# Optimization experiments

Measured on AMD Instinct MI355X. Metric: run time of the kernel, lower is better.

The kernel has to match this reference:

```python
import jax, jax.numpy as jnp
import numpy as np

TAU = 1.5
K = 4
EPS = 1e-5
GN_GROUPS = 8

def conv2d(x, w, pad, rhs_dilation=(1, 1)):
    return jax.lax.conv_general_dilated(
        x, w, window_strides=(1, 1),
        padding=[(pad, pad), (pad, pad)],
        rhs_dilation=rhs_dilation,
        dimension_numbers=("NCHW", "OIHW", "NCHW"))

def setup_inputs() -> dict:
    key = jax.random.key(0)
    ks = jax.random.split(key, 16)
    s = 0.05  # weight scale to keep activations sane
    B, C, H, W = 16, 128, 64, 64
    O, HID, CG, SE = 128, 32, 16, 16
    d = {}
    d["x"] = jax.random.normal(ks[0], (B, C, H, W), jnp.float32)
    d["base_weight"] = jax.random.normal(ks[1], (O, C, 3, 3), jnp.float32) * s
    d["delta_weight"] = jax.random.normal(ks[2], (K, O, C, 3, 3), jnp.float32) * s
    d["kernel_scale"] = jnp.ones((K, O, 1, 1, 1), jnp.float32)
    d["gc_w1"] = jax.random.normal(ks[3], (HID, C), jnp.float32) * s
    d["gc_w2"] = jax.random.normal(ks[4], (C, HID), jnp.float32) * s
    d["rc_w"] = jax.random.normal(ks[5], (HID, C, 3, 3), jnp.float32) * s
    d["bn_gamma"] = jnp.ones((HID,), jnp.float32)
    d["bn_beta"] = jnp.zeros((HID,), jnp.float32)
    d["bn_mean"] = jnp.zeros((HID,), jnp.float32)
    d["bn_var"] = jnp.ones((HID,), jnp.float32)
    d["rg_w"] = jax.random.normal(ks[6], (HID, C), jnp.float32) * s
    d["gate_w"] = jax.random.normal(ks[7], (K * O, HID), jnp.float32) * s
    d["gate_b"] = jnp.zeros((K * O,), jnp.float32)
    d["cg_w1"] = jax.random.normal(ks[8], (CG, C), jnp.float32) * s
    d["cg_b1"] = jnp.zeros((CG,), jnp.float32)
    d["cg_w2"] = jax.random.normal(ks[9], (C, CG), jnp.float32) * s
    d["cg_b2"] = jnp.zeros((C,), jnp.float32)
    d["sg_w"] = jax.random.normal(ks[10], (1, 2, 7, 7), jnp.float32) * s
    d["gn_gamma"] = jnp.ones((O,), jnp.float32)
    d["gn_beta"] = jnp.zeros((O,), jnp.float32)
    d["se_w1"] = jax.random.normal(ks[11], (SE, O), jnp.float32) * s
    d["se_b1"] = jnp.zeros((SE,), jnp.float32)
    d["se_w2"] = jax.random.normal(ks[12], (O, SE), jnp.float32) * s
    d["se_b2"] = jnp.zeros((O,), jnp.float32)
    d["identity_scale"] = jnp.float32(0.0)
    d["bias"] = jnp.zeros((O,), jnp.float32)
    return d

def reference(x, base_weight, delta_weight, kernel_scale, gc_w1, gc_w2, rc_w,
              bn_gamma, bn_beta, bn_mean, bn_var, rg_w, gate_w, gate_b,
              cg_w1, cg_b1, cg_w2, cg_b2, sg_w, gn_gamma, gn_beta,
              se_w1, se_b1, se_w2, se_b2, identity_scale, bias):
    identity = x
    B, C, H, W = x.shape
    O = base_weight.shape[0]

    # global context gate (squeeze-excite style)
    p = x.mean((2, 3))                                    # [B,C]
    g = jax.nn.sigmoid(jax.nn.silu(p @ gc_w1.T) @ gc_w2.T)
    x = x * g[:, :, None, None]

    # channel gate
    pc = x.mean((2, 3))
    c_attn = jax.nn.sigmoid(jax.nn.silu(pc @ cg_w1.T + cg_b1) @ cg_w2.T + cg_b2)
    # spatial gate
    s_in = jnp.concatenate([x.mean(1, keepdims=True), x.max(1, keepdims=True)], axis=1)
    s_attn = jax.nn.sigmoid(conv2d(s_in, sg_w, pad=3))
    x = x * c_attn[:, :, None, None] * s_attn

    # router: dilated conv + BN(eval) + SiLU, plus global branch
    lf = conv2d(x, rc_w, pad=2, rhs_dilation=(2, 2))
    lf = (lf - bn_mean[None, :, None, None]) * jax.lax.rsqrt(bn_var + EPS)[None, :, None, None]
    lf = lf * bn_gamma[None, :, None, None] + bn_beta[None, :, None, None]
    lf = jax.nn.silu(lf)
    gf = jax.nn.silu(x.mean((2, 3)) @ rg_w.T)             # [B,HID]
    lf = lf + gf[:, :, None, None]
    alpha = jnp.einsum("bhij,oh->boij", lf, gate_w) + gate_b[None, :, None, None]
    alpha = alpha.reshape(B, K, O, H, W)
    alpha = jax.nn.softmax(alpha / TAU, axis=1)

    # unfold (k=3, stride=1, pad=1, dilation=1) -> H_out=H, W_out=W
    xp = jnp.pad(x, ((0, 0), (0, 0), (1, 1), (1, 1)))
    patches = jnp.stack([xp[:, :, i:i + H, j:j + W]
                         for i in range(3) for j in range(3)], axis=2)  # [B,C,9,H,W]
    L = H * W
    xu = patches.reshape(B, C * 9, L).transpose(0, 2, 1)  # [B,L,C*9]

    base = base_weight.reshape(O, -1)
    delta = (delta_weight * kernel_scale).reshape(K, O, -1)
    # same-size bilinear resize of alpha is the identity
    alpha_map = alpha.reshape(B, K, O, L)

    static = jnp.einsum("blf,of->bol", xu, base)          # [B,O,L]
    res = jnp.einsum("blf,kof->bkol", xu, delta)          # [B,K,O,L]
    final = static + (res * alpha_map).sum(1)
    out = final.reshape(B, O, H, W)

    # GroupNorm
    go = out.reshape(B, GN_GROUPS, O // GN_GROUPS, H, W)
    mu = go.mean((2, 3, 4), keepdims=True)
    var = go.var((2, 3, 4), keepdims=True)
    out = ((go - mu) * jax.lax.rsqrt(var + EPS)).reshape(B, O, H, W)
    out = out * gn_gamma[None, :, None, None] + gn_beta[None, :, None, None]

    # output SE
    ps = out.mean((2, 3))
    se = jax.nn.sigmoid(jax.nn.silu(ps @ se_w1.T + se_b1) @ se_w2.T + se_b2)
    out = out * se[:, :, None, None]

    out = out + jnp.tanh(identity_scale) * identity
    out = out + bias[None, :, None, None]
    return out
```

## Files before the change

### kernel.cpp

```cpp
#include <hip/hip_runtime.h>
#include <hip/hip_bf16.h>
#include <math.h>

typedef __bf16 bf16_t;
typedef __bf16 bf16x8 __attribute__((ext_vector_type(8)));
typedef __bf16 bf16x4 __attribute__((ext_vector_type(4)));
typedef __bf16 bf16x2 __attribute__((ext_vector_type(2)));
typedef float  f32x4  __attribute__((ext_vector_type(4)));

#define EPSF 1e-5f
#define TAUF 1.5f

__device__ __forceinline__ float sigmoidf_(float x){ return 1.f/(1.f+__expf(-x)); }
__device__ __forceinline__ float siluf_(float x){ return x*sigmoidf_(x); }

__device__ __forceinline__ void gload_lds16(const void* g, void* l){
  __builtin_amdgcn_global_load_lds((const __attribute__((address_space(1))) unsigned int*)g,
                                   (__attribute__((address_space(3))) unsigned int*)l, 16, 0, 0);
}

__global__ void k_pool(const float* __restrict__ x, float* __restrict__ p){
  int bc = blockIdx.x; const float* xr = x + (size_t)bc*4096;
  float s = 0.f;
  for (int i = threadIdx.x; i < 4096; i += 256) s += xr[i];
  __shared__ float sb[4];
  for (int off=32; off; off>>=1) s += __shfl_down(s, off);
  if ((threadIdx.x & 63)==0) sb[threadIdx.x>>6] = s;
  __syncthreads();
  if (threadIdx.x==0) p[bc] = (sb[0]+sb[1]+sb[2]+sb[3]) * (1.f/4096.f);
}

__global__ void k_small1(const float* __restrict__ p, const float* __restrict__ gc_w1,
                         const float* __restrict__ gc_w2, const float* __restrict__ cg_w1,
                         const float* __restrict__ cg_b1, const float* __restrict__ cg_w2,
                         const float* __restrict__ cg_b2,
                         float* __restrict__ gbuf, float* __restrict__ gate){
  int b = blockIdx.x; int t = threadIdx.x;
  __shared__ float ps[128], h1[32], pc[128], c1[16];
  ps[t] = p[b*128+t];
  __syncthreads();
  if (t < 32){ float a=0.f; for(int c=0;c<128;c++) a += ps[c]*gc_w1[t*128+c]; h1[t]=siluf_(a); }
  __syncthreads();
  float a=0.f; for(int j=0;j<32;j++) a += h1[j]*gc_w2[t*32+j];
  float g = sigmoidf_(a);
  gbuf[b*128+t] = g; pc[t] = ps[t]*g;
  __syncthreads();
  if (t < 16){ float a2=cg_b1[t]; for(int c=0;c<128;c++) a2 += pc[c]*cg_w1[t*128+c]; c1[t]=siluf_(a2); }
  __syncthreads();
  float a3=cg_b2[t]; for(int j=0;j<16;j++) a3 += c1[j]*cg_w2[t*16+j];
  gate[b*128+t] = g * sigmoidf_(a3);
}

__global__ void k_spatial(const float* __restrict__ x, const float* __restrict__ gbuf,
                          float* __restrict__ sin_){
  int bi = blockIdx.x; int b = bi>>6; int h = bi&63;
  int wv = threadIdx.x>>6, w = threadIdx.x&63;
  __shared__ float psum[4][64], pmax[4][64];
  float sm=0.f, mx=-1e30f;
  const float* xb = x + (((size_t)b*128 + wv*32)*64 + h)*64 + w;
  const float* gb = gbuf + b*128 + wv*32;
  #pragma unroll 4
  for (int c=0;c<32;c++){
    float v = xb[(size_t)c*4096] * gb[c];
    sm += v; mx = fmaxf(mx, v);
  }
  psum[wv][w]=sm; pmax[wv][w]=mx;
  __syncthreads();
  if (threadIdx.x < 64){
    float s = psum[0][w]+psum[1][w]+psum[2][w]+psum[3][w];
    float m = fmaxf(fmaxf(pmax[0][w],pmax[1][w]),fmaxf(pmax[2][w],pmax[3][w]));
    sin_[b*8192 + h*64 + w]        = s*(1.f/128.f);
    sin_[b*8192 + 4096 + h*64 + w] = m;
  }
}

__global__ void k_zb(bf16_t* __restrict__ x2q){
  size_t base = (size_t)blockIdx.x*68*68*8;
  float4 z = {0.f,0.f,0.f,0.f};
  for (int i = threadIdx.x; i < 272; i += 256){
    int r = i/68; int wp = i - r*68;
    int hp = (r&1) + (r>>1)*66;
    *(float4*)(x2q + base + ((size_t)hp*68 + wp)*8) = z;
  }
  {
    int i = threadIdx.x;
    int hp = 2 + (i>>2);
    int wp = (i&1) + (i&2)*33;
    *(float4*)(x2q + base + ((size_t)hp*68 + wp)*8) = z;
  }
}

__global__ void k_x2(const float* __restrict__ x, const float* __restrict__ gate,
                     const float* __restrict__ sin_, const float* __restrict__ sg_w,
                     bf16_t* __restrict__ x2q, float* __restrict__ pc2){
  int bi = blockIdx.x; int b = bi>>6; int h = bi&63;
  __shared__ bf16_t tile[128*66];
  __shared__ float sh_sin[980];
  __shared__ float sh_sgw[98];
  __shared__ float satt_row[64];
  int tid = threadIdx.x, wv = tid>>6, lane = tid&63;
  for (int i=tid;i<980;i+=256){
    int c2 = i/490; int rr = i - c2*490; int r = rr/70; int k = rr - r*70;
    int hh = h + r - 3; int ww = k - 3;
    float v = 0.f;
    if (hh>=0 && hh<64 && ww>=0 && ww<64) v = sin_[b*8192 + c2*4096 + hh*64 + ww];
    sh_sin[i] = v;
  }
  if (tid < 98) sh_sgw[tid] = sg_w[tid];
  __syncthreads();
  if (tid < 64){
    float a = 0.f;
    #pragma unroll
    for (int c2=0;c2<2;c2++)
      #pragma unroll
      for (int r=0;r<7;r++)
        #pragma unroll
        for (int j=0;j<7;j++)
          a += sh_sin[c2*490 + r*70 + tid + j] * sh_sgw[c2*49 + r*7 + j];
    satt_row[tid] = sigmoidf_(a);
  }
  __syncthreads();
  float sa = satt_row[lane];
  for (int it=0; it<32; it++){
    int c = it*4 + wv;
    float v = x[(((size_t)(b*128+c))*64 + h)*64 + lane] * gate[b*128+c] * sa;
    tile[c*66 + lane] = (bf16_t)v;
    float s = v;
    for (int off=32; off; off>>=1) s += __shfl_down(s, off);
    if (lane==0) atomicAdd(&pc2[b*128+c], s);
  }
  __syncthreads();
  for (int it=0; it<4; it++){
    int idx = it*256 + tid;
    int cq = idx>>6; int w = idx&63;
    int c0 = cq*8;
    bf16x8 v;
    #pragma unroll
    for (int e=0;e<8;e++) v[e] = tile[(c0+e)*66 + w];
    *(bf16x8*)(x2q + (((((size_t)b*4 + (cq>>2))*4 + (cq&3))*68 + (h+2))*68 + (w+2))*8) = v;
  }
}

__global__ void k_small2(const float* __restrict__ pc2, const float* __restrict__ rg_w,
                         float* __restrict__ gf){
  int b = blockIdx.x; int t = threadIdx.x;
  if (t < 32){
    float a=0.f; for(int c=0;c<128;c++) a += pc2[b*128+c]*(1.f/4096.f)*rg_w[t*128+c];
    gf[b*32+t] = siluf_(a);
  }
}

__global__ void k_wprep(const float* __restrict__ base_w, const float* __restrict__ delta_w,
                        const float* __restrict__ kscale, const float* __restrict__ rc_w,
                        bf16_t* __restrict__ WCQ, bf16_t* __restrict__ RCWQ){
  int i = blockIdx.x*256 + threadIdx.x;
  if (i < 589824){
    int c8 = i&7; int o16 = (i>>3)&15; int q = (i>>7)&3; int s = (i>>9)&3;
    int h2 = (i>>11)&3; int r = i>>13; int t = r%9; int ob = r/9;
    int o = ob*16 + o16; int c = h2*32 + q*8 + c8;
    float v = base_w[(o*128+c)*9 + t] + delta_w[(((s*128)+o)*128 + c)*9 + t]*kscale[s*128+o];
    WCQ[i] = (bf16_t)v;
  } else if (i < 589824 + 36864){
    int j = i - 589824;
    int c8 = j&7; int h16 = (j>>3)&15; int q = (j>>7)&3; int n2 = (j>>9)&1;
    int r = j>>10; int t = r%9; int h2 = r/9;
    int hid = n2*16 + h16; int c = h2*32 + q*8 + c8;
    RCWQ[j] = (bf16_t)rc_w[(hid*128+c)*9 + t];
  }
}

__global__ void __launch_bounds__(256) k_router(
    const bf16_t* __restrict__ x2q, const bf16_t* __restrict__ RCWQ,
    const float* __restrict__ bn_gamma, const float* __restrict__ bn_beta,
    const float* __restrict__ bn_mean, const float* __restrict__ bn_var,
    const float* __restrict__ gf, bf16_t* __restrict__ lfb){
  __shared__ __align__(16) char smem[44544];
  int tid = threadIdx.x;
  int wv = tid>>6, lane = tid&63, m16 = lane&15, q = lane>>4;
  int rb = blockIdx.x & 31, b = blockIdx.x >> 5;
  int r0 = rb*2;
  int rloc = wv&1;
  int ws0 = (wv>>1)*2;

  f32x4 acc[2][2] = {};

  #pragma unroll 1
  for (int h2=0; h2<4; h2++){
    const char* asrc = (const char*)(x2q + ((((size_t)(b*4+h2)*4 + wv)*68 + r0)*68)*8);
    #pragma unroll
    for (int j=0;j<7;j++){
      if (j*64 + lane < 408)
        gload_lds16(asrc + j*1024 + lane*16, (char*)smem + wv*6528 + j*1024);
    }
    const char* wsrc = (const char*)(RCWQ + (size_t)h2*9216) + wv*4608;
    #pragma unroll
    for (int j=0;j<5;j++){
      if (j*64 + lane < 288)
        gload_lds16(wsrc + j*1024 + lane*16, (char*)smem + 26112 + wv*4608 + j*1024);
    }
    __syncthreads();
    #pragma unroll
    for (int t=0; t<9; t++){
      int di = t/3, dj = t - di*3;
      bf16x8 aw0 = *(const bf16x8*)((const char*)smem + 26112 + (t*2+0)*1024 + q*256 + m16*16);
      bf16x8 aw1 = *(const bf16x8*)((const char*)smem + 26112 + (t*2+1)*1024 + q*256 + m16*16);
      #pragma unroll
      for (int mt=0; mt<2; mt++){
        int wseg = ws0 + mt;
        bf16x8 bs = *(const bf16x8*)((const char*)smem + q*6528 +
                     ((rloc + 2*di)*68 + wseg*16 + m16 + 2*dj)*16);
        acc[0][mt] = __builtin_amdgcn_mfma_f32_16x16x32_bf16(aw0, bs, acc[0][mt], 0,0,0);
        acc[1][mt] = __builtin_amdgcn_mfma_f32_16x16x32_bf16(aw1, bs, acc[1][mt], 0,0,0);
      }
    }
    __syncthreads();
  }

  #pragma unroll
  for (int n2=0;n2<2;n2++){
    float aa[4], bb[4];
    #pragma unroll
    for (int i=0;i<4;i++){
      int hid = n2*16 + q*4 + i;
      float a = bn_gamma[hid]*rsqrtf(bn_var[hid]+EPSF);
      aa[i] = a;
      bb[i] = bn_beta[hid] - bn_mean[hid]*a;
    }
    #pragma unroll
    for (int mt=0;mt<2;mt++){
      bf16x4 yv;
      #pragma unroll
      for (int i=0;i<4;i++){
        int hid = n2*16 + q*4 + i;
        yv[i] = (bf16_t)(siluf_(aa[i]*acc[n2][mt][i] + bb[i]) + gf[b*32+hid]);
      }
      size_t pos = (size_t)b*4096 + (r0+rloc)*64 + (ws0+mt)*16 + m16;
      *(bf16x4*)(lfb + pos*32 + n2*16 + q*4) = yv;
    }
  }
}

__global__ void __launch_bounds__(256, 2) k_main(
    const bf16_t* __restrict__ x2q, const bf16_t* __restrict__ WCQ,
    const bf16_t* __restrict__ lfb, const float* __restrict__ gate_w,
    const float* __restrict__ gate_b, bf16_t* __restrict__ outp,
    float* __restrict__ csum, float* __restrict__ cssq){
  __shared__ __align__(16) char smem[80960];
  bf16_t* shGW  = (bf16_t*)(smem + 43584);
  float*  sred  = (float*)(smem + 80448);

  int tid = threadIdx.x;
  int wv = tid>>6, lane = tid&63, m16 = lane&15, q = lane>>4;
  int bx = blockIdx.x;
  int ob = bx >> 7; int rem = bx & 127; int b = rem >> 3; int hb = rem & 7;
  int h0 = hb*8, obase = ob*16;

  f32x4 acc[8][4] = {};

  int baseA[8];
  #pragma unroll
  for (int mi=0;mi<8;mi++){
    int row = wv*2 + (mi>>2); int wseg = mi&3;
    baseA[mi] = (row*68 + wseg*16 + m16 + 1)*16 + q*10896;
  }
  int baseB = q*256 + m16*16;

  #pragma unroll 1
  for (int h2=0; h2<4; h2++){
    const char* asrc = (const char*)(x2q + ((((size_t)(b*4+h2)*4 + wv)*68 + (h0+1))*68)*8);
    #pragma unroll
    for (int j=0;j<11;j++){
      if (j*64 + lane < 680)
        gload_lds16(asrc + j*1024 + lane*16, (char*)smem + wv*10896 + j*1024);
    }
    const char* bsrc = (const char*)WCQ + ((size_t)(ob*9)*4 + h2)*4096;
    #pragma unroll
    for (int j=0;j<9;j++)
      gload_lds16(bsrc + j*16384 + wv*1024 + lane*16,
                  (char*)smem + 43584 + j*4096 + wv*1024);
    __syncthreads();
    #pragma unroll
    for (int t=0; t<9; t++){
      int di = t/3, dj = t - di*3;
      int toff = (di*68 + dj)*16;
      bf16x8 av[8], bv[4];
      #pragma unroll
      for (int mi=0;mi<8;mi++) av[mi] = *(const bf16x8*)((const char*)smem + baseA[mi] + toff);
      #pragma unroll
      for (int s=0;s<4;s++)  bv[s] = *(const bf16x8*)((const char*)smem + 43584 + t*4096 + s*1024 + baseB);
      #pragma unroll
      for (int s=0;s<4;s++){
        #pragma unroll
        for (int mi=0;mi<8;mi++)
          acc[mi][s] = __builtin_amdgcn_mfma_f32_16x16x32_bf16(av[mi], bv[s], acc[mi][s], 0,0,0);
      }
    }
    __syncthreads();
  }

  const char* lfsrc = (const char*)(lfb + ((size_t)b*4096 + h0*64)*32);
  for (int i = wv; i < 32; i += 4)
    gload_lds16(lfsrc + i*1024 + lane*16, (char*)smem + i*1024);
  for (int idx = tid; idx < 2048; idx += 256){
    int n = idx>>5, j = idx&31;
    shGW[n*32+j] = (bf16_t)gate_w[((n>>4)*128 + obase + (n&15))*32 + j];
  }
  __syncthreads();

  bf16x8 bg[4];
  #pragma unroll
  for (int kk=0;kk<4;kk++) bg[kk] = *(const bf16x8*)((const char*)shGW + (kk*16+m16)*64 + q*16);
  float gb[4];
  #pragma unroll
  for (int kk=0;kk<4;kk++) gb[kk] = gate_b[kk*128 + obase + m16];

  const float itau = 1.f/TAUF;
  float s1 = 0.f, s2 = 0.f;
  size_t orow = ((size_t)(b*128 + obase + m16))*4096 + h0*64;
  #pragma unroll
  for (int mi=0; mi<8; mi++){
    bf16x8 avL = *(const bf16x8*)((const char*)smem + (wv*128 + mi*16 + m16)*64 + q*16);
    f32x4 zero = {};
    f32x4 lg[4];
    #pragma unroll
    for (int kk=0;kk<4;kk++)
      lg[kk] = __builtin_amdgcn_mfma_f32_16x16x32_bf16(avL, bg[kk], zero, 0,0,0);
    bf16x4 yv;
    #pragma unroll
    for (int r=0;r<4;r++){
      float l0 = (lg[0][r]+gb[0])*itau, l1 = (lg[1][r]+gb[1])*itau;
      float l2 = (lg[2][r]+gb[2])*itau, l3 = (lg[3][r]+gb[3])*itau;
      float mx = fmaxf(fmaxf(l0,l1),fmaxf(l2,l3));
      float e0=__expf(l0-mx), e1=__expf(l1-mx), e2=__expf(l2-mx), e3=__expf(l3-mx);
      float inv = 1.f/(e0+e1+e2+e3);
      float y = (e0*acc[mi][0][r] + e1*acc[mi][1][r]
               + e2*acc[mi][2][r] + e3*acc[mi][3][r])*inv;
      s1 += y; s2 += y*y;
      yv[r] = (bf16_t)y;
    }
    *(bf16x4*)(outp + orow + wv*128 + mi*16 + q*4) = yv;
  }

  s1 += __shfl_down(s1, 32); s1 += __shfl_down(s1, 16);
  s2 += __shfl_down(s2, 32); s2 += __shfl_down(s2, 16);
  if (lane < 16){ sred[wv*16 + lane] = s1; sred[64 + wv*16 + lane] = s2; }
  __syncthreads();
  if (tid < 16){
    float a = sred[tid] + sred[16+tid] + sred[32+tid] + sred[48+tid];
    float c = sred[64+tid] + sred[80+tid] + sred[96+tid] + sred[112+tid];
    atomicAdd(&csum[b*128 + obase + tid], a);
    atomicAdd(&cssq[b*128 + obase + tid], c);
  }
}

__global__ void k_small3(const float* __restrict__ csum, const float* __restrict__ cssq,
                         const float* __restrict__ gn_gamma, const float* __restrict__ gn_beta,
                         const float* __restrict__ se_w1, const float* __restrict__ se_b1,
                         const float* __restrict__ se_w2, const float* __restrict__ se_b2,
                         float* __restrict__ sca, float* __restrict__ shb){
  int b = blockIdx.x; int o = threadIdx.x;
  __shared__ float s1[128], s2[128], gmu[8], grs[8], psl[128], t1[16];
  s1[o] = csum[b*128+o]; s2[o] = cssq[b*128+o];
  __syncthreads();
  if (o<8){
    float a=0.f,a2=0.f; for(int j=0;j<16;j++){ a+=s1[o*16+j]; a2+=s2[o*16+j]; }
    float mu = a*(1.f/65536.f); float var = a2*(1.f/65536.f) - mu*mu;
    gmu[o]=mu; grs[o]=rsqrtf(var+EPSF);
  }
  __syncthreads();
  int g = o>>4;
  psl[o] = (s1[o]*(1.f/4096.f) - gmu[g])*grs[g]*gn_gamma[o] + gn_beta[o];
  __syncthreads();
  if (o<16){ float a = se_b1[o]; for(int c=0;c<128;c++) a += psl[c]*se_w1[o*128+c]; t1[o]=siluf_(a); }
  __syncthreads();
  float a = se_b2[o]; for(int j=0;j<16;j++) a += t1[j]*se_w2[o*16+j];
  float sev = sigmoidf_(a);
  sca[b*128+o] = grs[g]*gn_gamma[o]*sev;
  shb[b*128+o] = (gn_beta[o] - gmu[g]*grs[g]*gn_gamma[o])*sev;
}

__global__ void k_final(const bf16_t* __restrict__ outp, const float* __restrict__ x,
                        const float* __restrict__ sca, const float* __restrict__ shb,
                        const float* __restrict__ bias, const float* __restrict__ iscale,
                        float* __restrict__ out){
  float ts = tanhf(iscale[0]);
  size_t i = ((size_t)blockIdx.x*256 + threadIdx.x)*8;
  int bo = (int)(i>>12); int o = bo&127;
  float A = sca[bo], Bv = shb[bo] + bias[o];
  bf16x8 ov = *(const bf16x8*)(outp + i);
  float4 x0 = *(const float4*)(x+i), x1 = *(const float4*)(x+i+4);
  float4 r0, r1;
  r0.x = (float)ov[0]*A + Bv + ts*x0.x;
  r0.y = (float)ov[1]*A + Bv + ts*x0.y;
  r0.z = (float)ov[2]*A + Bv + ts*x0.z;
  r0.w = (float)ov[3]*A + Bv + ts*x0.w;
  r1.x = (float)ov[4]*A + Bv + ts*x1.x;
  r1.y = (float)ov[5]*A + Bv + ts*x1.y;
  r1.z = (float)ov[6]*A + Bv + ts*x1.z;
  r1.w = (float)ov[7]*A + Bv + ts*x1.w;
  *(float4*)(out+i) = r0; *(float4*)(out+i+4) = r1;
}

extern "C" void kernel_launch(void* const* d_in, const int* in_sizes, int n_in,
                              void* d_out, int out_size, void* d_ws, size_t ws_size,
                              hipStream_t stream){
  const float* x      = (const float*)d_in[0];
  const float* base_w = (const float*)d_in[1];
  const float* delta_w= (const float*)d_in[2];
  const float* kscale = (const float*)d_in[3];
  const float* gc_w1  = (const float*)d_in[4];
  const float* gc_w2  = (const float*)d_in[5];
  const float* rc_w   = (const float*)d_in[6];
  const float* bn_g   = (const float*)d_in[7];
  const float* bn_b   = (const float*)d_in[8];
  const float* bn_m   = (const float*)d_in[9];
  const float* bn_v   = (const float*)d_in[10];
  const float* rg_w   = (const float*)d_in[11];
  const float* gate_w = (const float*)d_in[12];
  const float* gate_b = (const float*)d_in[13];
  const float* cg_w1  = (const float*)d_in[14];
  const float* cg_b1  = (const float*)d_in[15];
  const float* cg_w2  = (const float*)d_in[16];
  const float* cg_b2  = (const float*)d_in[17];
  const float* sg_w   = (const float*)d_in[18];
  const float* gn_g   = (const float*)d_in[19];
  const float* gn_b   = (const float*)d_in[20];
  const float* se_w1  = (const float*)d_in[21];
  const float* se_b1  = (const float*)d_in[22];
  const float* se_w2  = (const float*)d_in[23];
  const float* se_b2  = (const float*)d_in[24];
  const float* iscale = (const float*)d_in[25];
  const float* bias   = (const float*)d_in[26];
  float* out = (float*)d_out;

  char* ws = (char*)d_ws;
  size_t off = 0;
  auto alloc = [&](size_t bytes)->void*{ void* p = ws + off; off += (bytes + 255) & ~(size_t)255; return p; };
  bf16_t* X2Q = (bf16_t*)alloc(16ull*4*4*68*68*8*2);
  bf16_t* WCQ = (bf16_t*)alloc(589824ull*2);
  bf16_t* RCWQ= (bf16_t*)alloc(36864ull*2);
  bf16_t* LF  = (bf16_t*)alloc(16ull*4096*32*2);
  bf16_t* OUTP= (bf16_t*)alloc(16ull*128*4096*2);
  float* PC2  = (float*)alloc(2048*4);
  float* CSUM = (float*)alloc(2048*4);
  float* CSSQ = (float*)alloc(2048*4);
  float* P    = (float*)alloc(2048*4);
  float* GB   = (float*)alloc(2048*4);
  float* GATE = (float*)alloc(2048*4);
  float* GF   = (float*)alloc(512*4);
  float* SIN  = (float*)alloc(16ull*8192*4);
  float* SCA  = (float*)alloc(2048*4);
  float* SHB  = (float*)alloc(2048*4);

  (void)hipMemsetAsync(PC2, 0, 3*8192, stream);

  k_wprep  <<<2448, 256, 0, stream>>>(base_w, delta_w, kscale, rc_w, WCQ, RCWQ);
  k_pool   <<<2048, 256, 0, stream>>>(x, P);
  k_small1 <<<16,   128, 0, stream>>>(P, gc_w1, gc_w2, cg_w1, cg_b1, cg_w2, cg_b2, GB, GATE);
  k_spatial<<<1024, 256, 0, stream>>>(x, GB, SIN);
  k_zb     <<<256,  256, 0, stream>>>(X2Q);
  k_x2     <<<1024, 256, 0, stream>>>(x, GATE, SIN, sg_w, X2Q, PC2);
  k_small2 <<<16,    64, 0, stream>>>(PC2, rg_w, GF);
  k_router <<<512,  256, 0, stream>>>(X2Q, RCWQ, bn_g, bn_b, bn_m, bn_v, GF, LF);
  k_main   <<<1024, 256, 0, stream>>>(X2Q, WCQ, LF, gate_w, gate_b, OUTP, CSUM, CSSQ);
  k_small3 <<<16,   128, 0, stream>>>(CSUM, CSSQ, gn_g, gn_b, se_w1, se_b1, se_w2, se_b2, SCA, SHB);
  k_final  <<<4096, 256, 0, stream>>>(OUTP, x, SCA, SHB, bias, iscale, out);
}
```

Baseline: 321.2 us.

## Fold border zeroing and router gate GEMV into neighbouring kernels

Removes two kernel launches. The padded-border zeroing moves into extra blocks of the weight-prep kernel, and the small pooled-feature GEMV plus SiLU is computed inside each router block from the pooled sums. k_x2 also now stages fp32 values in a padded LDS tile and computes per-channel row sums with one thread per channel, instead of a wave shuffle reduction and an atomic for every channel iteration. The cost is redundant GEMV work in all 512 router blocks and a serial 64-element sum per thread in k_x2.

```diff
diff --git a/kernel.cpp b/kernel.cpp
--- a/kernel.cpp
+++ b/kernel.cpp
@@ -5,7 +5,6 @@
 typedef __bf16 bf16_t;
 typedef __bf16 bf16x8 __attribute__((ext_vector_type(8)));
 typedef __bf16 bf16x4 __attribute__((ext_vector_type(4)));
-typedef __bf16 bf16x2 __attribute__((ext_vector_type(2)));
 typedef float  f32x4  __attribute__((ext_vector_type(4)));
 
 #define EPSF 1e-5f
@@ -74,27 +73,12 @@
   }
 }
 
-__global__ void k_zb(bf16_t* __restrict__ x2q){
-  size_t base = (size_t)blockIdx.x*68*68*8;
-  float4 z = {0.f,0.f,0.f,0.f};
-  for (int i = threadIdx.x; i < 272; i += 256){
-    int r = i/68; int wp = i - r*68;
-    int hp = (r&1) + (r>>1)*66;
-    *(float4*)(x2q + base + ((size_t)hp*68 + wp)*8) = z;
-  }
-  {
-    int i = threadIdx.x;
-    int hp = 2 + (i>>2);
-    int wp = (i&1) + (i&2)*33;
-    *(float4*)(x2q + base + ((size_t)hp*68 + wp)*8) = z;
-  }
-}
-
-__global__ void k_x2(const float* __restrict__ x, const float* __restrict__ gate,
-                     const float* __restrict__ sin_, const float* __restrict__ sg_w,
-                     bf16_t* __restrict__ x2q, float* __restrict__ pc2){
+__global__ void __launch_bounds__(256) k_x2(
+    const float* __restrict__ x, const float* __restrict__ gate,
+    const float* __restrict__ sin_, const float* __restrict__ sg_w,
+    bf16_t* __restrict__ x2q, float* __restrict__ pc2){
   int bi = blockIdx.x; int b = bi>>6; int h = bi&63;
-  __shared__ bf16_t tile[128*66];
+  __shared__ float tile[128*65];
   __shared__ float sh_sin[980];
   __shared__ float sh_sgw[98];
   __shared__ float satt_row[64];
@@ -121,14 +105,11 @@
   }
   __syncthreads();
   float sa = satt_row[lane];
-  for (int it=0; it<32; it++){
-    int c = it*4 + wv;
-    float v = x[(((size_t)(b*128+c))*64 + h)*64 + lane] * gate[b*128+c] * sa;
-    tile[c*66 + lane] = (bf16_t)v;
-    float s = v;
-    for (int off=32; off; off>>=1) s += __shfl_down(s, off);
-    if (lane==0) atomicAdd(&pc2[b*128+c], s);
-  }
+  const float* xb = x + (((size_t)b*128 + wv*32)*64 + h)*64 + lane;
+  const float* gb = gate + b*128 + wv*32;
+  #pragma unroll 8
+  for (int i=0;i<32;i++)
+    tile[(wv*32+i)*65 + lane] = xb[(size_t)i*4096] * gb[i] * sa;
   __syncthreads();
   for (int it=0; it<4; it++){
     int idx = it*256 + tid;
@@ -136,24 +117,41 @@
     int c0 = cq*8;
     bf16x8 v;
     #pragma unroll
-    for (int e=0;e<8;e++) v[e] = tile[(c0+e)*66 + w];
+    for (int e=0;e<8;e++) v[e] = (bf16_t)tile[(c0+e)*65 + w];
     *(bf16x8*)(x2q + (((((size_t)b*4 + (cq>>2))*4 + (cq&3))*68 + (h+2))*68 + (w+2))*8) = v;
   }
-}
-
-__global__ void k_small2(const float* __restrict__ pc2, const float* __restrict__ rg_w,
-                         float* __restrict__ gf){
-  int b = blockIdx.x; int t = threadIdx.x;
-  if (t < 32){
-    float a=0.f; for(int c=0;c<128;c++) a += pc2[b*128+c]*(1.f/4096.f)*rg_w[t*128+c];
-    gf[b*32+t] = siluf_(a);
+  if (tid < 128){
+    const float* row = &tile[tid*65];
+    float s = 0.f;
+    #pragma unroll 8
+    for (int w=0;w<64;w++) s += row[w];
+    atomicAdd(&pc2[b*128+tid], s);
   }
 }
 
 __global__ void k_wprep(const float* __restrict__ base_w, const float* __restrict__ delta_w,
                         const float* __restrict__ kscale, const float* __restrict__ rc_w,
-                        bf16_t* __restrict__ WCQ, bf16_t* __restrict__ RCWQ){
-  int i = blockIdx.x*256 + threadIdx.x;
+                        bf16_t* __restrict__ WCQ, bf16_t* __restrict__ RCWQ,
+                        bf16_t* __restrict__ x2q){
+  int bx = blockIdx.x;
+  if (bx >= 2448){
+    int p = bx - 2448;
+    size_t base = (size_t)p*68*68*8;
+    float4 z = {0.f,0.f,0.f,0.f};
+    for (int i = threadIdx.x; i < 272; i += 256){
+      int r = i/68; int wp = i - r*68;
+      int hp = (r&1) + (r>>1)*66;
+      *(float4*)(x2q + base + ((size_t)hp*68 + wp)*8) = z;
+    }
+    {
+      int i = threadIdx.x;
+      int hp = 2 + (i>>2);
+      int wp = (i&1) + (i&2)*33;
+      *(float4*)(x2q + base + ((size_t)hp*68 + wp)*8) = z;
+    }
+    return;
+  }
+  int i = bx*256 + threadIdx.x;
   if (i < 589824){
     int c8 = i&7; int o16 = (i>>3)&15; int q = (i>>7)&3; int s = (i>>9)&3;
     int h2 = (i>>11)&3; int r = i>>13; int t = r%9; int ob = r/9;
@@ -173,8 +171,11 @@
     const bf16_t* __restrict__ x2q, const bf16_t* __restrict__ RCWQ,
     const float* __restrict__ bn_gamma, const float* __restrict__ bn_beta,
     const float* __restrict__ bn_mean, const float* __restrict__ bn_var,
-    const float* __restrict__ gf, bf16_t* __restrict__ lfb){
+    const float* __restrict__ pc2, const float* __restrict__ rg_w,
+    bf16_t* __restrict__ lfb){
   __shared__ __align__(16) char smem[44544];
+  __shared__ float sgf[32];
+  __shared__ float spart[256];
   int tid = threadIdx.x;
   int wv = tid>>6, lane = tid&63, m16 = lane&15, q = lane>>4;
   int rb = blockIdx.x & 31, b = blockIdx.x >> 5;
@@ -182,6 +183,14 @@
   int rloc = wv&1;
   int ws0 = (wv>>1)*2;
 
+  {
+    int hid = tid&31, seg = tid>>5;
+    float a=0.f;
+    #pragma unroll
+    for (int j=0;j<16;j++) a += pc2[b*128 + seg*16 + j]*rg_w[hid*128 + seg*16 + j];
+    spart[tid] = a;
+  }
+
   f32x4 acc[2][2] = {};
 
   #pragma unroll 1
@@ -199,6 +208,12 @@
         gload_lds16(wsrc + j*1024 + lane*16, (char*)smem + 26112 + wv*4608 + j*1024);
     }
     __syncthreads();
+    if (h2==0 && tid < 32){
+      float s = 0.f;
+      #pragma unroll
+      for (int k=0;k<8;k++) s += spart[k*32+tid];
+      sgf[tid] = siluf_(s*(1.f/4096.f));
+    }
     #pragma unroll
     for (int t=0; t<9; t++){
       int di = t/3, dj = t - di*3;
@@ -232,7 +247,7 @@
       #pragma unroll
       for (int i=0;i<4;i++){
         int hid = n2*16 + q*4 + i;
-        yv[i] = (bf16_t)(siluf_(aa[i]*acc[n2][mt][i] + bb[i]) + gf[b*32+hid]);
+        yv[i] = (bf16_t)(siluf_(aa[i]*acc[n2][mt][i] + bb[i]) + sgf[hid]);
       }
       size_t pos = (size_t)b*4096 + (r0+rloc)*64 + (ws0+mt)*16 + m16;
       *(bf16x4*)(lfb + pos*32 + n2*16 + q*4) = yv;
@@ -447,21 +462,18 @@
   float* P    = (float*)alloc(2048*4);
   float* GB   = (float*)alloc(2048*4);
   float* GATE = (float*)alloc(2048*4);
-  float* GF   = (float*)alloc(512*4);
   float* SIN  = (float*)alloc(16ull*8192*4);
   float* SCA  = (float*)alloc(2048*4);
   float* SHB  = (float*)alloc(2048*4);
 
   (void)hipMemsetAsync(PC2, 0, 3*8192, stream);
 
-  k_wprep  <<<2448, 256, 0, stream>>>(base_w, delta_w, kscale, rc_w, WCQ, RCWQ);
+  k_wprep  <<<2704, 256, 0, stream>>>(base_w, delta_w, kscale, rc_w, WCQ, RCWQ, X2Q);
   k_pool   <<<2048, 256, 0, stream>>>(x, P);
   k_small1 <<<16,   128, 0, stream>>>(P, gc_w1, gc_w2, cg_w1, cg_b1, cg_w2, cg_b2, GB, GATE);
   k_spatial<<<1024, 256, 0, stream>>>(x, GB, SIN);
-  k_zb     <<<256,  256, 0, stream>>>(X2Q);
   k_x2     <<<1024, 256, 0, stream>>>(x, GATE, SIN, sg_w, X2Q, PC2);
-  k_small2 <<<16,    64, 0, stream>>>(PC2, rg_w, GF);
-  k_router <<<512,  256, 0, stream>>>(X2Q, RCWQ, bn_g, bn_b, bn_m, bn_v, GF, LF);
+  k_router <<<512,  256, 0, stream>>>(X2Q, RCWQ, bn_g, bn_b, bn_m, bn_v, PC2, rg_w, LF);
   k_main   <<<1024, 256, 0, stream>>>(X2Q, WCQ, LF, gate_w, gate_b, OUTP, CSUM, CSSQ);
   k_small3 <<<16,   128, 0, stream>>>(CSUM, CSSQ, gn_g, gn_b, se_w1, se_b1, se_w2, se_b2, SCA, SHB);
   k_final  <<<4096, 256, 0, stream>>>(OUTP, x, SCA, SHB, bias, iscale, out);
```

Result: faster. 258.5 us (-19.5%).
